# Kernel optimization log

Hardware: AMD Instinct MI355X
Metric: run time of the kernel (lower is better)

Reference implementation:

```python
import jax, jax.numpy as jnp
import numpy as np

NH = 16

def sinusoidal_pos(pos, nh=NH):
    # pos: [B, L] -> P: [B, L, nh], interleaved sin/cos with integer multiples of pi
    freqs = jnp.arange(1, nh // 2 + 1, dtype=pos.dtype) * jnp.pi  # [nh/2]
    ang = pos[..., None] * freqs                                   # [B, L, nh/2]
    # interleave: even channels sin, odd channels cos
    P = jnp.stack([jnp.sin(ang), jnp.cos(ang)], axis=-1)           # [B, L, nh/2, 2]
    return P.reshape(*pos.shape, nh)


def setup_inputs() -> dict:
    key = jax.random.key(0)
    k1, k2, k3, k4, k5, k6 = jax.random.split(key, 6)
    B, L, nx, nh = 2048, 1024, 8, NH
    return {
        "x": jax.random.normal(k1, (B, L, nx), dtype=jnp.float32),
        "pos": jax.random.uniform(k2, (B, L), dtype=jnp.float32),
        "W_q": jax.random.normal(k3, (nh, nx), dtype=jnp.float32) * 0.1,
        "W_k": jax.random.normal(k4, (nh, nx), dtype=jnp.float32) * 0.1,
        "W_v": jax.random.normal(k5, (nh, nx), dtype=jnp.float32) * 0.1,
        "W_o": jax.random.normal(k6, (nh, nh), dtype=jnp.float32) * 0.1,
    }


def reference(x, pos, W_q, W_k, W_v, W_o):
    # x: [B, L, nx]; pos: [B, L]; Linear weights are [out, in] (torch convention)
    q = jnp.einsum("blx,hx->blh", x, W_q)
    k = jnp.einsum("blx,hx->blh", x, W_k)
    v = jnp.einsum("blx,hx->blh", x, W_v)
    P = sinusoidal_pos(pos, W_q.shape[0])
    q = q + P
    k = k + P
    L = q.shape[1]
    # channel-wise attention: score over feature dim, [B, nh, nh]
    score = jnp.einsum("bld,ble->bde", q, k) / jnp.sqrt(jnp.asarray(L, q.dtype))
    attn = jax.nn.softmax(score, axis=-1)
    out = jnp.einsum("bde,ble->bdl", attn, v)   # [B, nh, L]
    out = jnp.einsum("bdl,hd->blh", out, W_o)   # transpose then W_o: [B, L, nh]
    return out
```

## Files before the change

### kernel.cpp

```cpp
#include <hip/hip_runtime.h>
#include <cstdint>
#include <cstddef>

#define LSEQ 1024
#define NH   16
#define NX   8

__device__ __forceinline__ uint32_t f2bf(float f) {
    uint32_t u = __float_as_uint(f);
    u += 0x7fffu + ((u >> 16) & 1u);
    return u >> 16;
}
__device__ __forceinline__ float bflo(uint32_t w) { return __uint_as_float(w << 16); }
__device__ __forceinline__ float bfhi(uint32_t w) { return __uint_as_float(w & 0xffff0000u); }

__global__ __launch_bounds__(256, 1)
void attn_fused_kernel(const float* __restrict__ x, const float* __restrict__ pos,
                       const float* __restrict__ Wq, const float* __restrict__ Wk,
                       const float* __restrict__ Wv, const float* __restrict__ Wo,
                       float* __restrict__ out) {
    __shared__ __align__(16) char smem_raw[65536];
    uint16_t* q_lds = (uint16_t*)smem_raw;
    uint16_t* k_lds = (uint16_t*)(smem_raw + 32768);
    float* scorebuf = (float*)smem_raw;
    float* attn_s   = (float*)(smem_raw + 4096);
    float* M_s      = (float*)(smem_raw + 5120);
    float* weff_s   = (float*)(smem_raw + 6144);

    const int tid = threadIdx.x;
    const int b   = blockIdx.x;
    const float* xb = x   + (size_t)b * LSEQ * NX;
    const float* pb = pos + (size_t)b * LSEQ;

    {
        const int dg   = tid >> 6;
        const int lidx = tid & 63;
        float wq[4][8], wk[4][8];
        #pragma unroll
        for (int r = 0; r < 4; ++r) {
            const float4 a0 = *(const float4*)(Wq + (4 * dg + r) * 8);
            const float4 a1 = *(const float4*)(Wq + (4 * dg + r) * 8 + 4);
            const float4 b0 = *(const float4*)(Wk + (4 * dg + r) * 8);
            const float4 b1 = *(const float4*)(Wk + (4 * dg + r) * 8 + 4);
            wq[r][0]=a0.x; wq[r][1]=a0.y; wq[r][2]=a0.z; wq[r][3]=a0.w;
            wq[r][4]=a1.x; wq[r][5]=a1.y; wq[r][6]=a1.z; wq[r][7]=a1.w;
            wk[r][0]=b0.x; wk[r][1]=b0.y; wk[r][2]=b0.z; wk[r][3]=b0.w;
            wk[r][4]=b1.x; wk[r][5]=b1.y; wk[r][6]=b1.z; wk[r][7]=b1.w;
        }
        const float f0 = (float)(2 * dg + 1);
        const float f1 = (float)(2 * dg + 2);
        for (int p = 0; p < 16; ++p) {
            const int l = p * 64 + lidx;
            const float4 xa = *(const float4*)(xb + (size_t)l * 8);
            const float4 xc = *(const float4*)(xb + (size_t)l * 8 + 4);
            const float pv = pb[l];
            float pe[4];
            pe[0] = sinpif(pv * f0); pe[1] = cospif(pv * f0);
            pe[2] = sinpif(pv * f1); pe[3] = cospif(pv * f1);
            float qv[4], kv[4];
            #pragma unroll
            for (int r = 0; r < 4; ++r) {
                qv[r] = xa.x*wq[r][0] + xa.y*wq[r][1] + xa.z*wq[r][2] + xa.w*wq[r][3]
                      + xc.x*wq[r][4] + xc.y*wq[r][5] + xc.z*wq[r][6] + xc.w*wq[r][7] + pe[r];
                kv[r] = xa.x*wk[r][0] + xa.y*wk[r][1] + xa.z*wk[r][2] + xa.w*wk[r][3]
                      + xc.x*wk[r][4] + xc.y*wk[r][5] + xc.z*wk[r][6] + xc.w*wk[r][7] + pe[r];
            }
            uint2 qp, kp;
            qp.x = f2bf(qv[0]) | (f2bf(qv[1]) << 16);
            qp.y = f2bf(qv[2]) | (f2bf(qv[3]) << 16);
            kp.x = f2bf(kv[0]) | (f2bf(kv[1]) << 16);
            kp.y = f2bf(kv[2]) | (f2bf(kv[3]) << 16);
            *(uint2*)(q_lds + (size_t)l * 16 + 4 * dg) = qp;
            *(uint2*)(k_lds + (size_t)l * 16 + 4 * dg) = kp;
        }
    }
    __syncthreads();

    {
        const int lg = tid >> 4;
        const int dt = (tid >> 2) & 3;
        const int et = tid & 3;
        float acc[4][4];
        #pragma unroll
        for (int i = 0; i < 4; ++i)
            #pragma unroll
            for (int j = 0; j < 4; ++j) acc[i][j] = 0.f;

        const uint16_t* qp = q_lds + lg * 16 + dt * 4;
        const uint16_t* kp = k_lds + lg * 16 + et * 4;
        #pragma unroll 4
        for (int i = 0; i < 64; ++i) {
            const uint2 qw = *(const uint2*)(qp + i * 256);
            const uint2 kw = *(const uint2*)(kp + i * 256);
            const float q0 = bflo(qw.x), q1 = bfhi(qw.x), q2 = bflo(qw.y), q3 = bfhi(qw.y);
            const float k0 = bflo(kw.x), k1 = bfhi(kw.x), k2 = bflo(kw.y), k3 = bfhi(kw.y);
            acc[0][0] += q0*k0; acc[0][1] += q0*k1; acc[0][2] += q0*k2; acc[0][3] += q0*k3;
            acc[1][0] += q1*k0; acc[1][1] += q1*k1; acc[1][2] += q1*k2; acc[1][3] += q1*k3;
            acc[2][0] += q2*k0; acc[2][1] += q2*k1; acc[2][2] += q2*k2; acc[2][3] += q2*k3;
            acc[3][0] += q3*k0; acc[3][1] += q3*k1; acc[3][2] += q3*k2; acc[3][3] += q3*k3;
        }
        #pragma unroll
        for (int di = 0; di < 4; ++di)
            #pragma unroll
            for (int ei = 0; ei < 4; ++ei) {
                acc[di][ei] += __shfl_xor(acc[di][ei], 16);
                acc[di][ei] += __shfl_xor(acc[di][ei], 32);
            }
        __syncthreads();
        const int lane = tid & 63;
        const int w    = tid >> 6;
        if (lane < 16) {
            #pragma unroll
            for (int di = 0; di < 4; ++di)
                #pragma unroll
                for (int ei = 0; ei < 4; ++ei)
                    scorebuf[w * 256 + (dt * 4 + di) * 16 + (et * 4 + ei)] = acc[di][ei];
        }
    }
    __syncthreads();

    {
        const int e = tid & 15;
        float s = scorebuf[tid] + scorebuf[256 + tid] + scorebuf[512 + tid] + scorebuf[768 + tid];
        s *= 0.03125f;
        float mx = s;
        #pragma unroll
        for (int m = 1; m < 16; m <<= 1) mx = fmaxf(mx, __shfl_xor(mx, m));
        const float ex = __expf(s - mx);
        float sum = ex;
        #pragma unroll
        for (int m = 1; m < 16; m <<= 1) sum += __shfl_xor(sum, m);
        attn_s[tid] = ex / sum;
        __syncthreads();

        const int h = tid >> 4;
        float acc = 0.f;
        #pragma unroll
        for (int d = 0; d < 16; ++d) acc += Wo[h * 16 + d] * attn_s[d * 16 + e];
        M_s[h * 16 + e] = acc;
        __syncthreads();

        if (tid < 128) {
            const int hh = tid >> 3, xc = tid & 7;
            float wv = 0.f;
            #pragma unroll
            for (int ee = 0; ee < 16; ++ee) wv += M_s[hh * 16 + ee] * Wv[ee * 8 + xc];
            weff_s[hh * 8 + xc] = wv;
        }
    }
    __syncthreads();

    {
        float xr[4][8];
        #pragma unroll
        for (int r = 0; r < 4; ++r) {
            const int l = tid + 256 * r;
            const float4 a = *(const float4*)(xb + (size_t)l * 8);
            const float4 c = *(const float4*)(xb + (size_t)l * 8 + 4);
            xr[r][0]=a.x; xr[r][1]=a.y; xr[r][2]=a.z; xr[r][3]=a.w;
            xr[r][4]=c.x; xr[r][5]=c.y; xr[r][6]=c.z; xr[r][7]=c.w;
        }
        float o[4][16];
        #pragma unroll
        for (int h = 0; h < 16; ++h) {
            const float4 wA = *(const float4*)(weff_s + h * 8);
            const float4 wB = *(const float4*)(weff_s + h * 8 + 4);
            #pragma unroll
            for (int r = 0; r < 4; ++r) {
                o[r][h] = xr[r][0]*wA.x + xr[r][1]*wA.y + xr[r][2]*wA.z + xr[r][3]*wA.w
                        + xr[r][4]*wB.x + xr[r][5]*wB.y + xr[r][6]*wB.z + xr[r][7]*wB.w;
            }
        }
        #pragma unroll
        for (int r = 0; r < 4; ++r) {
            const size_t base = ((size_t)b * LSEQ + tid + 256 * r) * NH;
            #pragma unroll
            for (int g = 0; g < 4; ++g) {
                *(float4*)(out + base + g * 4) =
                    make_float4(o[r][g*4+0], o[r][g*4+1], o[r][g*4+2], o[r][g*4+3]);
            }
        }
    }
}

extern "C" void kernel_launch(void* const* d_in, const int* in_sizes, int n_in,
                              void* d_out, int out_size, void* d_ws, size_t ws_size,
                              hipStream_t stream) {
    const float* x   = (const float*)d_in[0];
    const float* pos = (const float*)d_in[1];
    const float* Wq  = (const float*)d_in[2];
    const float* Wk  = (const float*)d_in[3];
    const float* Wv  = (const float*)d_in[4];
    const float* Wo  = (const float*)d_in[5];
    float* out = (float*)d_out;
    const int B = in_sizes[1] / LSEQ;
    attn_fused_kernel<<<B, 256, 0, stream>>>(x, pos, Wq, Wk, Wv, Wo, out);
}
```

Baseline: 97.68 us.

## Replace Q/K materialization with moment-based score computation in single-wave blocks

Instead of building bf16 Q and K in LDS and running a 16x16 reduction over the sequence, each thread accumulates sequence moments: the second moments of x, the cross-moments of x with sin/cos harmonics, and sums of harmonics up to frequency 16. Harmonics come from a Chebyshev recurrence seeded by one sinpif/cospif. The score matrix is then assembled algebraically using product-to-sum identities. The block shrinks to 64 threads with 196 accumulator registers plus an LDS transpose-reduction, which risks register pressure and low occupancy.

New measurement: 247.4 us. +153.2%, slower.

```diff
diff --git a/kernel.cpp b/kernel.cpp
--- a/kernel.cpp
+++ b/kernel.cpp
@@ -5,181 +5,195 @@
 #define LSEQ 1024
 #define NH   16
 #define NX   8
-
-__device__ __forceinline__ uint32_t f2bf(float f) {
-    uint32_t u = __float_as_uint(f);
-    u += 0x7fffu + ((u >> 16) & 1u);
-    return u >> 16;
-}
-__device__ __forceinline__ float bflo(uint32_t w) { return __uint_as_float(w << 16); }
-__device__ __forceinline__ float bfhi(uint32_t w) { return __uint_as_float(w & 0xffff0000u); }
-
-__global__ __launch_bounds__(256, 1)
-void attn_fused_kernel(const float* __restrict__ x, const float* __restrict__ pos,
-                       const float* __restrict__ Wq, const float* __restrict__ Wk,
-                       const float* __restrict__ Wv, const float* __restrict__ Wo,
-                       float* __restrict__ out) {
-    __shared__ __align__(16) char smem_raw[65536];
-    uint16_t* q_lds = (uint16_t*)smem_raw;
-    uint16_t* k_lds = (uint16_t*)(smem_raw + 32768);
-    float* scorebuf = (float*)smem_raw;
-    float* attn_s   = (float*)(smem_raw + 4096);
-    float* M_s      = (float*)(smem_raw + 5120);
-    float* weff_s   = (float*)(smem_raw + 6144);
-
-    const int tid = threadIdx.x;
-    const int b   = blockIdx.x;
+#define NACC 196
+
+__global__ __launch_bounds__(64, 2)
+void attn_moments(const float* __restrict__ x, const float* __restrict__ pos,
+                  const float* __restrict__ Wq, const float* __restrict__ Wk,
+                  const float* __restrict__ Wv, const float* __restrict__ Wo,
+                  float* __restrict__ out) {
+    __shared__ __align__(16) float red[64 * 65];
+    __shared__ float sums[256];
+    float* score_s = red;
+    float* attn_s  = red + 256;
+    float* M_s     = red + 512;
+    float* U_s     = red + 768;
+    float* weff_s  = red + 896;
+
+    const int lane = threadIdx.x;
+    const int b    = blockIdx.x;
     const float* xb = x   + (size_t)b * LSEQ * NX;
     const float* pb = pos + (size_t)b * LSEQ;
 
-    {
-        const int dg   = tid >> 6;
-        const int lidx = tid & 63;
-        float wq[4][8], wk[4][8];
-        #pragma unroll
-        for (int r = 0; r < 4; ++r) {
-            const float4 a0 = *(const float4*)(Wq + (4 * dg + r) * 8);
-            const float4 a1 = *(const float4*)(Wq + (4 * dg + r) * 8 + 4);
-            const float4 b0 = *(const float4*)(Wk + (4 * dg + r) * 8);
-            const float4 b1 = *(const float4*)(Wk + (4 * dg + r) * 8 + 4);
-            wq[r][0]=a0.x; wq[r][1]=a0.y; wq[r][2]=a0.z; wq[r][3]=a0.w;
-            wq[r][4]=a1.x; wq[r][5]=a1.y; wq[r][6]=a1.z; wq[r][7]=a1.w;
-            wk[r][0]=b0.x; wk[r][1]=b0.y; wk[r][2]=b0.z; wk[r][3]=b0.w;
-            wk[r][4]=b1.x; wk[r][5]=b1.y; wk[r][6]=b1.z; wk[r][7]=b1.w;
-        }
-        const float f0 = (float)(2 * dg + 1);
-        const float f1 = (float)(2 * dg + 2);
-        for (int p = 0; p < 16; ++p) {
-            const int l = p * 64 + lidx;
-            const float4 xa = *(const float4*)(xb + (size_t)l * 8);
-            const float4 xc = *(const float4*)(xb + (size_t)l * 8 + 4);
-            const float pv = pb[l];
-            float pe[4];
-            pe[0] = sinpif(pv * f0); pe[1] = cospif(pv * f0);
-            pe[2] = sinpif(pv * f1); pe[3] = cospif(pv * f1);
-            float qv[4], kv[4];
+    float A[NACC];
+    #pragma unroll
+    for (int i = 0; i < NACC; ++i) A[i] = 0.f;
+
+    float4 xa = *(const float4*)(xb + (size_t)lane * 8);
+    float4 xc = *(const float4*)(xb + (size_t)lane * 8 + 4);
+    float  pv = pb[lane];
+    for (int i = 0; i < 16; ++i) {
+        float4 nxa = xa, nxc = xc; float npv = pv;
+        if (i < 15) {
+            const int l = (i + 1) * 64 + lane;
+            nxa = *(const float4*)(xb + (size_t)l * 8);
+            nxc = *(const float4*)(xb + (size_t)l * 8 + 4);
+            npv = pb[l];
+        }
+        const float px[8] = {xa.x, xa.y, xa.z, xa.w, xc.x, xc.y, xc.z, xc.w};
+
+        {
+            int idx = 0;
             #pragma unroll
-            for (int r = 0; r < 4; ++r) {
-                qv[r] = xa.x*wq[r][0] + xa.y*wq[r][1] + xa.z*wq[r][2] + xa.w*wq[r][3]
-                      + xc.x*wq[r][4] + xc.y*wq[r][5] + xc.z*wq[r][6] + xc.w*wq[r][7] + pe[r];
-                kv[r] = xa.x*wk[r][0] + xa.y*wk[r][1] + xa.z*wk[r][2] + xa.w*wk[r][3]
-                      + xc.x*wk[r][4] + xc.y*wk[r][5] + xc.z*wk[r][6] + xc.w*wk[r][7] + pe[r];
+            for (int p = 0; p < 8; ++p)
+                #pragma unroll
+                for (int q = p; q < 8; ++q) { A[idx] += px[p] * px[q]; ++idx; }
+        }
+        {
+            const float s1 = sinpif(pv), c1 = cospif(pv);
+            const float c1x2 = 2.f * c1;
+            float s = s1, c = c1;
+            float s_p = 0.f, c_p = 1.f;
+            #pragma unroll
+            for (int m = 1; m <= 16; ++m) {
+                if (m > 1) {
+                    const float s_n = c1x2 * s - s_p;
+                    const float c_n = c1x2 * c - c_p;
+                    s_p = s; c_p = c; s = s_n; c = c_n;
+                }
+                if (m <= 8) {
+                    #pragma unroll
+                    for (int ch = 0; ch < 8; ++ch) {
+                        A[36 + ch * 16 + 2 * (m - 1)] += px[ch] * s;
+                        A[36 + ch * 16 + 2 * m - 1]   += px[ch] * c;
+                    }
+                }
+                A[163 + m] += s;
+                A[179 + m] += c;
             }
-            uint2 qp, kp;
-            qp.x = f2bf(qv[0]) | (f2bf(qv[1]) << 16);
-            qp.y = f2bf(qv[2]) | (f2bf(qv[3]) << 16);
-            kp.x = f2bf(kv[0]) | (f2bf(kv[1]) << 16);
-            kp.y = f2bf(kv[2]) | (f2bf(kv[3]) << 16);
-            *(uint2*)(q_lds + (size_t)l * 16 + 4 * dg) = qp;
-            *(uint2*)(k_lds + (size_t)l * 16 + 4 * dg) = kp;
-        }
-    }
-    __syncthreads();
-
-    {
-        const int lg = tid >> 4;
-        const int dt = (tid >> 2) & 3;
-        const int et = tid & 3;
-        float acc[4][4];
-        #pragma unroll
-        for (int i = 0; i < 4; ++i)
+        }
+        xa = nxa; xc = nxc; pv = npv;
+    }
+
+    #pragma unroll
+    for (int q = 0; q < 4; ++q) {
+        #pragma unroll
+        for (int v = 0; v < 64; ++v) {
+            const int a = q * 64 + v;
+            red[v * 65 + lane] = (a < NACC) ? A[a] : 0.f;
+        }
+        __syncthreads();
+        float t = 0.f;
+        const float* rp = red + lane * 65;
+        #pragma unroll 8
+        for (int r = 0; r < 64; ++r) t += rp[r];
+        if (q * 64 + lane < 256) sums[q * 64 + lane] = t;
+        __syncthreads();
+    }
+
+    #pragma unroll
+    for (int k = 0; k < 2; ++k) {
+        const int u = lane * 2 + k;
+        const int d = u >> 3, y = u & 7;
+        float acc = 0.f;
+        #pragma unroll
+        for (int xx = 0; xx < 8; ++xx) {
+            const int p = xx < y ? xx : y;
+            const int q = xx < y ? y : xx;
+            acc += Wq[d * 8 + xx] * sums[8 * p - (p * (p - 1)) / 2 + (q - p)];
+        }
+        U_s[u] = acc;
+    }
+    __syncthreads();
+
+    const float* Cs = sums + 36;
+    #pragma unroll
+    for (int k = 0; k < 4; ++k) {
+        const int idx = lane * 4 + k;
+        const int d = idx >> 4, e = idx & 15;
+        float a1 = 0.f, a2 = 0.f, a3 = 0.f;
+        #pragma unroll
+        for (int y = 0; y < 8; ++y) a1 += U_s[d * 8 + y] * Wk[e * 8 + y];
+        #pragma unroll
+        for (int xx = 0; xx < 8; ++xx) {
+            a2 += Wq[d * 8 + xx] * Cs[xx * 16 + e];
+            a3 += Wk[e * 8 + xx] * Cs[xx * 16 + d];
+        }
+        const int fi = (d >> 1) + 1, fj = (e >> 1) + 1;
+        const int sp = fi + fj;
+        const int sm = fi > fj ? fi - fj : fj - fi;
+        const float Smp = sums[163 + sp];
+        const float Cmp = sums[179 + sp];
+        const float Sms = (sm == 0) ? 0.f : sums[163 + sm];
+        const float Cms = (sm == 0) ? (float)LSEQ : sums[179 + sm];
+        const bool de = !(d & 1), ee = !(e & 1);
+        float Dv;
+        if (de && ee)       Dv = 0.5f * (Cms - Cmp);
+        else if (de && !ee) Dv = 0.5f * (Smp + (fi >= fj ? 1.f : -1.f) * Sms);
+        else if (!de && ee) Dv = 0.5f * (Smp + (fj >= fi ? 1.f : -1.f) * Sms);
+        else                Dv = 0.5f * (Cms + Cmp);
+        score_s[idx] = (a1 + a2 + a3 + Dv) * 0.03125f;
+    }
+    __syncthreads();
+
+    if (lane < 16) {
+        float mx = -1e30f;
+        #pragma unroll
+        for (int e = 0; e < 16; ++e) mx = fmaxf(mx, score_s[lane * 16 + e]);
+        float ex[16], sum = 0.f;
+        #pragma unroll
+        for (int e = 0; e < 16; ++e) { ex[e] = __expf(score_s[lane * 16 + e] - mx); sum += ex[e]; }
+        const float inv = 1.f / sum;
+        #pragma unroll
+        for (int e = 0; e < 16; ++e) attn_s[lane * 16 + e] = ex[e] * inv;
+    }
+    __syncthreads();
+
+    #pragma unroll
+    for (int k = 0; k < 4; ++k) {
+        const int idx = lane * 4 + k;
+        const int h = idx >> 4, e = idx & 15;
+        float acc = 0.f;
+        #pragma unroll
+        for (int d = 0; d < 16; ++d) acc += Wo[h * 16 + d] * attn_s[d * 16 + e];
+        M_s[idx] = acc;
+    }
+    __syncthreads();
+
+    #pragma unroll
+    for (int k = 0; k < 2; ++k) {
+        const int idx = lane * 2 + k;
+        const int h = idx >> 3, xx = idx & 7;
+        float acc = 0.f;
+        #pragma unroll
+        for (int e = 0; e < 16; ++e) acc += M_s[h * 16 + e] * Wv[e * 8 + xx];
+        weff_s[idx] = acc;
+    }
+    __syncthreads();
+
+    float Wr[128];
+    #pragma unroll
+    for (int k = 0; k < 32; ++k) {
+        const float4 t4 = *(const float4*)(weff_s + k * 4);
+        Wr[k * 4 + 0] = t4.x; Wr[k * 4 + 1] = t4.y; Wr[k * 4 + 2] = t4.z; Wr[k * 4 + 3] = t4.w;
+    }
+    for (int i = 0; i < 16; ++i) {
+        const int l = i * 64 + lane;
+        const float4 a = *(const float4*)(xb + (size_t)l * 8);
+        const float4 c = *(const float4*)(xb + (size_t)l * 8 + 4);
+        const float xr[8] = {a.x, a.y, a.z, a.w, c.x, c.y, c.z, c.w};
+        float o[16];
+        #pragma unroll
+        for (int h = 0; h < 16; ++h) {
+            float acc = 0.f;
             #pragma unroll
-            for (int j = 0; j < 4; ++j) acc[i][j] = 0.f;
-
-        const uint16_t* qp = q_lds + lg * 16 + dt * 4;
-        const uint16_t* kp = k_lds + lg * 16 + et * 4;
-        #pragma unroll 4
-        for (int i = 0; i < 64; ++i) {
-            const uint2 qw = *(const uint2*)(qp + i * 256);
-            const uint2 kw = *(const uint2*)(kp + i * 256);
-            const float q0 = bflo(qw.x), q1 = bfhi(qw.x), q2 = bflo(qw.y), q3 = bfhi(qw.y);
-            const float k0 = bflo(kw.x), k1 = bfhi(kw.x), k2 = bflo(kw.y), k3 = bfhi(kw.y);
-            acc[0][0] += q0*k0; acc[0][1] += q0*k1; acc[0][2] += q0*k2; acc[0][3] += q0*k3;
-            acc[1][0] += q1*k0; acc[1][1] += q1*k1; acc[1][2] += q1*k2; acc[1][3] += q1*k3;
-            acc[2][0] += q2*k0; acc[2][1] += q2*k1; acc[2][2] += q2*k2; acc[2][3] += q2*k3;
-            acc[3][0] += q3*k0; acc[3][1] += q3*k1; acc[3][2] += q3*k2; acc[3][3] += q3*k3;
-        }
-        #pragma unroll
-        for (int di = 0; di < 4; ++di)
-            #pragma unroll
-            for (int ei = 0; ei < 4; ++ei) {
-                acc[di][ei] += __shfl_xor(acc[di][ei], 16);
-                acc[di][ei] += __shfl_xor(acc[di][ei], 32);
-            }
-        __syncthreads();
-        const int lane = tid & 63;
-        const int w    = tid >> 6;
-        if (lane < 16) {
-            #pragma unroll
-            for (int di = 0; di < 4; ++di)
-                #pragma unroll
-                for (int ei = 0; ei < 4; ++ei)
-                    scorebuf[w * 256 + (dt * 4 + di) * 16 + (et * 4 + ei)] = acc[di][ei];
-        }
-    }
-    __syncthreads();
-
-    {
-        const int e = tid & 15;
-        float s = scorebuf[tid] + scorebuf[256 + tid] + scorebuf[512 + tid] + scorebuf[768 + tid];
-        s *= 0.03125f;
-        float mx = s;
-        #pragma unroll
-        for (int m = 1; m < 16; m <<= 1) mx = fmaxf(mx, __shfl_xor(mx, m));
-        const float ex = __expf(s - mx);
-        float sum = ex;
-        #pragma unroll
-        for (int m = 1; m < 16; m <<= 1) sum += __shfl_xor(sum, m);
-        attn_s[tid] = ex / sum;
-        __syncthreads();
-
-        const int h = tid >> 4;
-        float acc = 0.f;
-        #pragma unroll
-        for (int d = 0; d < 16; ++d) acc += Wo[h * 16 + d] * attn_s[d * 16 + e];
-        M_s[h * 16 + e] = acc;
-        __syncthreads();
-
-        if (tid < 128) {
-            const int hh = tid >> 3, xc = tid & 7;
-            float wv = 0.f;
-            #pragma unroll
-            for (int ee = 0; ee < 16; ++ee) wv += M_s[hh * 16 + ee] * Wv[ee * 8 + xc];
-            weff_s[hh * 8 + xc] = wv;
-        }
-    }
-    __syncthreads();
-
-    {
-        float xr[4][8];
-        #pragma unroll
-        for (int r = 0; r < 4; ++r) {
-            const int l = tid + 256 * r;
-            const float4 a = *(const float4*)(xb + (size_t)l * 8);
-            const float4 c = *(const float4*)(xb + (size_t)l * 8 + 4);
-            xr[r][0]=a.x; xr[r][1]=a.y; xr[r][2]=a.z; xr[r][3]=a.w;
-            xr[r][4]=c.x; xr[r][5]=c.y; xr[r][6]=c.z; xr[r][7]=c.w;
-        }
-        float o[4][16];
-        #pragma unroll
-        for (int h = 0; h < 16; ++h) {
-            const float4 wA = *(const float4*)(weff_s + h * 8);
-            const float4 wB = *(const float4*)(weff_s + h * 8 + 4);
-            #pragma unroll
-            for (int r = 0; r < 4; ++r) {
-                o[r][h] = xr[r][0]*wA.x + xr[r][1]*wA.y + xr[r][2]*wA.z + xr[r][3]*wA.w
-                        + xr[r][4]*wB.x + xr[r][5]*wB.y + xr[r][6]*wB.z + xr[r][7]*wB.w;
-            }
-        }
-        #pragma unroll
-        for (int r = 0; r < 4; ++r) {
-            const size_t base = ((size_t)b * LSEQ + tid + 256 * r) * NH;
-            #pragma unroll
-            for (int g = 0; g < 4; ++g) {
-                *(float4*)(out + base + g * 4) =
-                    make_float4(o[r][g*4+0], o[r][g*4+1], o[r][g*4+2], o[r][g*4+3]);
-            }
-        }
+            for (int xx = 0; xx < 8; ++xx) acc += xr[xx] * Wr[h * 8 + xx];
+            o[h] = acc;
+        }
+        const size_t base = ((size_t)b * LSEQ + l) * NH;
+        #pragma unroll
+        for (int g = 0; g < 4; ++g)
+            *(float4*)(out + base + g * 4) = make_float4(o[g*4+0], o[g*4+1], o[g*4+2], o[g*4+3]);
     }
 }
 
@@ -194,5 +208,5 @@
     const float* Wo  = (const float*)d_in[5];
     float* out = (float*)d_out;
     const int B = in_sizes[1] / LSEQ;
-    attn_fused_kernel<<<B, 256, 0, stream>>>(x, pos, Wq, Wk, Wv, Wo, out);
+    attn_moments<<<B, 64, 0, stream>>>(x, pos, Wq, Wk, Wv, Wo, out);
 }
```
